# Performance work log

Measured on AMD Instinct MI355X. Metric: run time of the kernel, lower is better.

The kernel has to match this reference:

```python
import jax, jax.numpy as jnp
import numpy as np

H = 3584        # hidden_size
NH = 16         # num_attention_heads
HD = 256        # head_dim
NKV = 8         # num_key_value_heads
GROUPS = NH // NKV
B, S = 2, 2048
SOFTCAP = 50.0
SCALE = 256.0 ** -0.5   # query_pre_attn_scalar ** -0.5
ROPE_BASE = 10000.0
NEG = -1e9


def _rotate_half(x):
    x1, x2 = jnp.split(x, 2, axis=-1)
    return jnp.concatenate([-x2, x1], axis=-1)


def _apply_rope(x, cos, sin):
    # x: [b, h, s, d]; cos/sin: [s, d]
    return x * cos[None, None] + _rotate_half(x) * sin[None, None]


def setup_inputs() -> dict:
    key = jax.random.key(0)
    k1, k2, k3, k4, k5 = jax.random.split(key, 5)
    hidden_states = jax.random.normal(k1, (B, S, H), dtype=jnp.float32)
    # additive causal mask [1, 1, S, S]
    causal = jnp.tril(jnp.ones((S, S), dtype=bool))
    attention_mask = jnp.where(causal, 0.0, NEG).astype(jnp.float32)[None, None]
    Wq = jax.random.normal(k2, (H, NH * HD), dtype=jnp.float32) * 0.02
    Wk = jax.random.normal(k3, (H, NKV * HD), dtype=jnp.float32) * 0.02
    Wv = jax.random.normal(k4, (H, NKV * HD), dtype=jnp.float32) * 0.02
    Wo = jax.random.normal(k5, (NH * HD, H), dtype=jnp.float32) * 0.02
    return {"hidden_states": hidden_states, "attention_mask": attention_mask,
            "Wq": Wq, "Wk": Wk, "Wv": Wv, "Wo": Wo}


def reference(hidden_states, attention_mask, Wq, Wk, Wv, Wo):
    b, s, _ = hidden_states.shape
    q = (hidden_states @ Wq).reshape(b, s, NH, HD).transpose(0, 2, 1, 3)   # [b,nh,s,d]
    k = (hidden_states @ Wk).reshape(b, s, NKV, HD).transpose(0, 2, 1, 3)  # [b,nkv,s,d]
    v = (hidden_states @ Wv).reshape(b, s, NKV, HD).transpose(0, 2, 1, 3)

    # RoPE (HF-style: freqs duplicated, rotate_half)
    pos = jnp.arange(s, dtype=jnp.float32)
    inv_freq = 1.0 / (ROPE_BASE ** (jnp.arange(0, HD, 2, dtype=jnp.float32) / HD))
    freqs = pos[:, None] * inv_freq[None, :]          # [s, d/2]
    emb = jnp.concatenate([freqs, freqs], axis=-1)    # [s, d]
    cos, sin = jnp.cos(emb), jnp.sin(emb)
    q = _apply_rope(q, cos, sin)
    k = _apply_rope(k, cos, sin)

    # repeat_kv for GQA
    k = jnp.repeat(k, GROUPS, axis=1)  # [b,nh,s,d]
    v = jnp.repeat(v, GROUPS, axis=1)

    scores = jnp.einsum('bhsd,bhtd->bhst', q, k) * SCALE
    # tanh logit softcapping
    scores = jnp.tanh(scores / SOFTCAP) * SOFTCAP
    scores = scores + attention_mask
    probs = jax.nn.softmax(scores.astype(jnp.float32), axis=-1).astype(q.dtype)
    out = jnp.einsum('bhst,bhtd->bhsd', probs, v)
    out = out.transpose(0, 2, 1, 3).reshape(b, s, NH * HD)
    return out @ Wo
```

## Files before the change

kernel.cpp:

```cpp
#include <hip/hip_runtime.h>
#include <cstdint>
#include <cstddef>

typedef __bf16 bf16x8 __attribute__((ext_vector_type(8)));
typedef unsigned short u16x8 __attribute__((ext_vector_type(8)));
typedef float  f32x4  __attribute__((ext_vector_type(4)));
typedef unsigned short u16;

#define GLDS16(GP, LP) __builtin_amdgcn_global_load_lds( \
    (const __attribute__((address_space(1))) void*)(GP), \
    (__attribute__((address_space(3))) void*)(LP), 16, 0, 0)

__device__ __forceinline__ float b2f(u16 u) {
  unsigned int x = ((unsigned int)u) << 16;
  return __builtin_bit_cast(float, x);
}
__device__ __forceinline__ u16 f2b(float f) {
  unsigned int u = __builtin_bit_cast(unsigned int, f);
  unsigned int r = (u + 0x7fffu + ((u >> 16) & 1u)) >> 16;
  return (u16)r;
}

constexpr int Bc  = 2;
constexpr int Sc  = 2048;
constexpr int Hc  = 3584;
constexpr int NHc = 16;
constexpr int HDc = 256;
constexpr int NKV = 8;
constexpr int QD  = NHc * HDc;
constexpr int QS  = 8192;
constexpr float SCALE   = 0.0625f;
constexpr float CAP     = 50.0f;
constexpr float INV_CAP = 1.0f / 50.0f;

__device__ __forceinline__ float softcap(float raw) {
  float y = raw * (SCALE * INV_CAP);
  float a = __builtin_fabsf(y);
  float e = __expf(-2.0f * a);
  float t = (1.0f - e) * __builtin_amdgcn_rcpf(1.0f + e);
  return copysignf(t, y) * CAP;
}

__global__ void rope_table_k(float* __restrict__ cosT, float* __restrict__ sinT) {
  int idx = blockIdx.x * 256 + threadIdx.x;
  int s = idx >> 7, i = idx & 127;
  float inv = expf((float)i * -0.0719557841560639f);
  float ang = (float)s * inv;
  cosT[idx] = cosf(ang);
  sinT[idx] = sinf(ang);
}

__global__ void cvt_f32_bf16(const float4* __restrict__ in, ushort4* __restrict__ out, int n4) {
  int i = blockIdx.x * 256 + threadIdx.x;
  int st = gridDim.x * 256;
  for (; i < n4; i += st) {
    float4 v = in[i];
    ushort4 u;
    u.x = f2b(v.x); u.y = f2b(v.y); u.z = f2b(v.z); u.w = f2b(v.w);
    out[i] = u;
  }
}

__global__ void transpose_cvt(const float* __restrict__ in, u16* __restrict__ out, int R, int C) {
  __shared__ float t[32][33];
  int c0 = blockIdx.x * 32, r0 = blockIdx.y * 32;
  int tx = threadIdx.x, ty = threadIdx.y;
#pragma unroll
  for (int i = 0; i < 4; i++)
    t[ty + i * 8][tx] = in[(size_t)(r0 + ty + i * 8) * C + c0 + tx];
  __syncthreads();
#pragma unroll
  for (int i = 0; i < 4; i++)
    out[(size_t)(c0 + ty + i * 8) * R + r0 + tx] = f2b(t[tx][ty + i * 8]);
}

__global__ void transpose_v(const u16* __restrict__ QKV, u16* __restrict__ Vt) {
  __shared__ u16 t[32][33];
  int b = blockIdx.z >> 3, kvh = blockIdx.z & 7;
  int s0 = blockIdx.x * 32, d0 = blockIdx.y * 32;
  int tx = threadIdx.x, ty = threadIdx.y;
#pragma unroll
  for (int i = 0; i < 4; i++)
    t[ty + i * 8][tx] = QKV[(size_t)(b * Sc + s0 + ty + i * 8) * QS + 6144 + kvh * HDc + d0 + tx];
  __syncthreads();
#pragma unroll
  for (int i = 0; i < 4; i++)
    Vt[(size_t)((b * NKV + kvh) * HDc + d0 + ty + i * 8) * Sc + s0 + tx] = t[tx][ty + i * 8];
}

template <int NH>
__global__ void rope_apply(u16* __restrict__ X, const float* __restrict__ cosT,
                           const float* __restrict__ sinT) {
  constexpr int LS = (NH == 16) ? 4 : 3;
  int idx = blockIdx.x * 256 + threadIdx.x;
  const int i4 = (idx & 31) << 2;
  const int h = (idx >> 5) & (NH - 1);
  const int row = idx >> (5 + LS);
  const int s = row & (Sc - 1);
  u16* p = X + (size_t)row * QS + h * 256 + i4;
  ushort4 lo = *(const ushort4*)p;
  ushort4 hi = *(const ushort4*)(p + 128);
  float4 c = *(const float4*)(cosT + s * 128 + i4);
  float4 sn = *(const float4*)(sinT + s * 128 + i4);
  ushort4 nlo, nhi;
  { float xl = b2f(lo.x), xh = b2f(hi.x);
    nlo.x = f2b(xl * c.x - xh * sn.x); nhi.x = f2b(xh * c.x + xl * sn.x); }
  { float xl = b2f(lo.y), xh = b2f(hi.y);
    nlo.y = f2b(xl * c.y - xh * sn.y); nhi.y = f2b(xh * c.y + xl * sn.y); }
  { float xl = b2f(lo.z), xh = b2f(hi.z);
    nlo.z = f2b(xl * c.z - xh * sn.z); nhi.z = f2b(xh * c.z + xl * sn.z); }
  { float xl = b2f(lo.w), xh = b2f(hi.w);
    nlo.w = f2b(xl * c.w - xh * sn.w); nhi.w = f2b(xh * c.w + xl * sn.w); }
  *(ushort4*)p = nlo;
  *(ushort4*)(p + 128) = nhi;
}

template <typename OT>
__global__ __launch_bounds__(512, 1) void gemm256(const u16* __restrict__ A,
                                                  const u16* __restrict__ Bt,
                                                  OT* __restrict__ C,
                                                  int M, int N, int K, int GM) {
  __shared__ alignas(16) u16 As[2][256 * 64];
  __shared__ alignas(16) u16 Bs[2][256 * 64];
  const int nwg = gridDim.x;
  const int cpx = nwg >> 3;
  const int wgid = (blockIdx.x & 7) * cpx + (blockIdx.x >> 3);
  const int GN = nwg / GM;
  const int width = 8 * GN;
  const int grp = wgid / width;
  const int rem = wgid - grp * width;
  const int m0 = (grp * 8 + (rem & 7)) * 256;
  const int n0 = (rem >> 3) * 256;
  const int tid = threadIdx.x;
  const int lane = tid & 63;
  const int w = tid >> 6;
  const int wm = w >> 2, wn = w & 3;
  const int lg = lane >> 4, lr = lane & 15;
  const int nkt = K >> 6;

  auto STAGE = [&](int buf, int kt) {
    const int k0 = kt * 64;
#pragma unroll
    for (int i = 0; i < 4; i++) {
      int c = i * 512 + tid;
      int row = c >> 3, slot = c & 7;
      GLDS16(A + (size_t)(m0 + row) * K + k0 + (slot ^ (row & 7)) * 8,
             (char*)As[buf] + c * 16);
    }
#pragma unroll
    for (int i = 0; i < 4; i++) {
      int c = i * 512 + tid;
      int row = c >> 3, slot = c & 7;
      GLDS16(Bt + (size_t)(n0 + row) * K + k0 + (slot ^ (row & 7)) * 8,
             (char*)Bs[buf] + c * 16);
    }
  };

  f32x4 acc[8][4] = {};

  STAGE(0, 0);
  STAGE(1, 1);
  asm volatile("s_waitcnt vmcnt(8)" ::: "memory");
  __builtin_amdgcn_sched_barrier(0);
  __builtin_amdgcn_s_barrier();

  for (int kt = 0; kt < nkt; ++kt) {
    const int buf = kt & 1;
    bf16x8 bfr[4][2], af[4][2], af2[4][2];
#pragma unroll
    for (int j = 0; j < 4; j++)
#pragma unroll
      for (int ks = 0; ks < 2; ks++) {
        int row = wn * 64 + j * 16 + lr;
        bfr[j][ks] = *(const bf16x8*)&Bs[buf][row * 64 + ((ks * 4 + lg) ^ (row & 7)) * 8];
      }
#pragma unroll
    for (int i = 0; i < 4; i++)
#pragma unroll
      for (int ks = 0; ks < 2; ks++) {
        int row = wm * 128 + i * 16 + lr;
        af[i][ks] = *(const bf16x8*)&As[buf][row * 64 + ((ks * 4 + lg) ^ (row & 7)) * 8];
      }
#pragma unroll
    for (int i = 0; i < 4; i++)
#pragma unroll
      for (int ks = 0; ks < 2; ks++) {
        int row = wm * 128 + 64 + i * 16 + lr;
        af2[i][ks] = *(const bf16x8*)&As[buf][row * 64 + ((ks * 4 + lg) ^ (row & 7)) * 8];
      }
    __builtin_amdgcn_s_setprio(1);
#pragma unroll
    for (int i = 0; i < 4; i++)
#pragma unroll
      for (int j = 0; j < 4; j++)
#pragma unroll
        for (int ks = 0; ks < 2; ks++)
          acc[i][j] = __builtin_amdgcn_mfma_f32_16x16x32_bf16(
              af[i][ks], bfr[j][ks], acc[i][j], 0, 0, 0);
    __builtin_amdgcn_s_setprio(0);
    asm volatile("s_waitcnt vmcnt(0) lgkmcnt(0)" ::: "memory");
    __builtin_amdgcn_sched_barrier(0);
    __builtin_amdgcn_s_barrier();
    if (kt + 2 < nkt) STAGE(buf, kt + 2);
    __builtin_amdgcn_s_setprio(1);
#pragma unroll
    for (int i = 0; i < 4; i++)
#pragma unroll
      for (int j = 0; j < 4; j++)
#pragma unroll
        for (int ks = 0; ks < 2; ks++)
          acc[4 + i][j] = __builtin_amdgcn_mfma_f32_16x16x32_bf16(
              af2[i][ks], bfr[j][ks], acc[4 + i][j], 0, 0, 0);
    __builtin_amdgcn_s_setprio(0);
  }

#pragma unroll
  for (int i = 0; i < 8; i++) {
    const int row = m0 + wm * 128 + i * 16 + lg * 4;
#pragma unroll
    for (int j = 0; j < 4; j++) {
      const int col = n0 + wn * 64 + j * 16 + lr;
#pragma unroll
      for (int r = 0; r < 4; r++) {
        if constexpr (sizeof(OT) == 2)
          C[(size_t)(row + r) * N + col] = f2b(acc[i][j][r]);
        else
          C[(size_t)(row + r) * N + col] = acc[i][j][r];
      }
    }
  }
}

__global__ __launch_bounds__(512) void attn_fwd(const u16* __restrict__ QKV,
                                                const u16* __restrict__ Vt,
                                                const float* __restrict__ cosT,
                                                const float* __restrict__ sinT,
                                                u16* __restrict__ AO) {
  constexpr int KVB = 32;
  __shared__ alignas(16) u16 Ks[2][KVB * 256];
  __shared__ alignas(16) u16 Vs[2][256 * KVB];
  __shared__ alignas(16) u16 Ps[8][16][40];
  const int bx = blockIdx.x, h = blockIdx.y, b = blockIdx.z;
  const int qt = b ? (15 - bx) : bx;
  const int q0 = qt * 128;
  const int kvh = h >> 1;
  const int tid = threadIdx.x, w = tid >> 6, lane = tid & 63;
  const int lg = lane >> 4, lr = lane & 15;
  const int myrow = q0 + w * 16 + lr;

  u16x8 qr[8];
  {
    const u16* qp = QKV + (size_t)(b * Sc + myrow) * QS + h * HDc + lg * 8;
#pragma unroll
    for (int kk = 0; kk < 8; kk++) qr[kk] = *(const u16x8*)(qp + kk * 32);
    const float* ct = cosT + myrow * 128 + lg * 8;
    const float* st = sinT + myrow * 128 + lg * 8;
#pragma unroll
    for (int kk = 0; kk < 4; kk++)
#pragma unroll
      for (int q4 = 0; q4 < 2; q4++) {
        float4 c = *(const float4*)(ct + kk * 32 + q4 * 4);
        float4 s = *(const float4*)(st + kk * 32 + q4 * 4);
#pragma unroll
        for (int e = 0; e < 4; e++) {
          int ei = q4 * 4 + e;
          float cc = (&c.x)[e], ss = (&s.x)[e];
          float lo = b2f(qr[kk][ei]), hi = b2f(qr[kk + 4][ei]);
          qr[kk][ei]     = f2b(lo * cc - hi * ss);
          qr[kk + 4][ei] = f2b(hi * cc + lo * ss);
        }
      }
  }
  bf16x8 qf[8];
#pragma unroll
  for (int kk = 0; kk < 8; kk++) qf[kk] = __builtin_bit_cast(bf16x8, qr[kk]);

  f32x4 o[16] = {};
  float m_r[4], l_r[4];
#pragma unroll
  for (int r = 0; r < 4; r++) { m_r[r] = -1e30f; l_r[r] = 0.0f; }
  const int my_qrow = q0 + w * 16 + lg * 4;
  const int wave_min_row = q0 + w * 16;
  const int wave_max_row = q0 + w * 16 + 15;

  const u16* kbase = QKV + (size_t)(b * Sc) * QS + 4096 + kvh * HDc;
  const u16* vbase = Vt + (size_t)((b * NKV + kvh) * HDc) * Sc;

  auto STAGE = [&](int buf, int t0) {
#pragma unroll
    for (int i = 0; i < 2; i++) {
      int c = i * 512 + tid;
      int row = c >> 5, slot = c & 31;
      GLDS16(kbase + (size_t)(t0 + row) * QS + (slot ^ (row & 7)) * 8,
             (char*)Ks[buf] + c * 16);
    }
#pragma unroll
    for (int i = 0; i < 2; i++) {
      int c = i * 512 + tid;
      int d = c >> 2, slot = c & 3;
      GLDS16(vbase + (size_t)d * Sc + t0 + (slot ^ (d & 3)) * 8,
             (char*)Vs[buf] + c * 16);
    }
  };

  const int nt = 4 * qt + 4;
  int cur = 0;
  STAGE(0, 0);
  for (int ti = 0; ti < nt; ++ti) {
    const int t0 = ti * 32;
    if (ti + 1 < nt) {
      STAGE(cur ^ 1, t0 + 32);
      asm volatile("s_waitcnt vmcnt(4)" ::: "memory");
    } else {
      asm volatile("s_waitcnt vmcnt(0)" ::: "memory");
    }
    __builtin_amdgcn_sched_barrier(0);
    __builtin_amdgcn_s_barrier();

    if (t0 <= wave_max_row) {
      const u16* KsT = Ks[cur];
      const u16* VsT = Vs[cur];

      f32x4 sc[2];
#pragma unroll
      for (int j = 0; j < 2; j++) {
        f32x4 a = {0.f, 0.f, 0.f, 0.f};
        const int row = j * 16 + lr;
#pragma unroll
        for (int kk = 0; kk < 8; kk++) {
          int s0 = (kk * 4 + lg) ^ (lr & 7);
          bf16x8 kf = *(const bf16x8*)&KsT[row * 256 + s0 * 8];
          a = __builtin_amdgcn_mfma_f32_16x16x32_bf16(qf[kk], kf, a, 0, 0, 0);
        }
        sc[j] = a;
      }

      float tmax[4] = {-1e30f, -1e30f, -1e30f, -1e30f};
      if (t0 + 31 > wave_min_row) {
#pragma unroll
        for (int j = 0; j < 2; j++)
#pragma unroll
          for (int r = 0; r < 4; r++) {
            float x = softcap(sc[j][r]);
            if (t0 + j * 16 + lr > my_qrow + r) x = -1e9f;
            sc[j][r] = x;
            tmax[r] = fmaxf(tmax[r], x);
          }
      } else {
#pragma unroll
        for (int j = 0; j < 2; j++)
#pragma unroll
          for (int r = 0; r < 4; r++) {
            float x = softcap(sc[j][r]);
            sc[j][r] = x;
            tmax[r] = fmaxf(tmax[r], x);
          }
      }
#pragma unroll
      for (int xm = 1; xm < 16; xm <<= 1)
#pragma unroll
        for (int r = 0; r < 4; r++) tmax[r] = fmaxf(tmax[r], __shfl_xor(tmax[r], xm, 64));

      bool need = false;
#pragma unroll
      for (int r = 0; r < 4; r++) need |= (tmax[r] > m_r[r] + 8.0f);
      if (__any(need)) {
        float scal[4];
#pragma unroll
        for (int r = 0; r < 4; r++) {
          float mn = fmaxf(m_r[r], tmax[r]);
          scal[r] = __expf(m_r[r] - mn);
          m_r[r] = mn;
          l_r[r] *= scal[r];
        }
#pragma unroll
        for (int df = 0; df < 16; df++)
#pragma unroll
          for (int r = 0; r < 4; r++) o[df][r] *= scal[r];
      }

      float psum[4] = {0.f, 0.f, 0.f, 0.f};
#pragma unroll
      for (int j = 0; j < 2; j++)
#pragma unroll
        for (int r = 0; r < 4; r++) {
          float p = __expf(sc[j][r] - m_r[r]);
          psum[r] += p;
          Ps[w][lg * 4 + r][j * 16 + lr] = f2b(p);
        }
#pragma unroll
      for (int xm = 1; xm < 16; xm <<= 1)
#pragma unroll
        for (int r = 0; r < 4; r++) psum[r] += __shfl_xor(psum[r], xm, 64);
#pragma unroll
      for (int r = 0; r < 4; r++) l_r[r] += psum[r];

      bf16x8 pf = *(const bf16x8*)&Ps[w][lr][lg * 8];
#pragma unroll
      for (int df = 0; df < 16; df++) {
        const int d = df * 16 + lr;
        int s0 = lg ^ (d & 3);
        bf16x8 vf = *(const bf16x8*)&VsT[d * KVB + s0 * 8];
        o[df] = __builtin_amdgcn_mfma_f32_16x16x32_bf16(pf, vf, o[df], 0, 0, 0);
      }
    }

    __builtin_amdgcn_s_barrier();
    cur ^= 1;
  }

  float inv_l[4];
#pragma unroll
  for (int r = 0; r < 4; r++) inv_l[r] = 1.0f / l_r[r];
  u16* op = AO + (size_t)(b * Sc + my_qrow) * QD + h * HDc + lr;
#pragma unroll
  for (int df = 0; df < 16; df++)
#pragma unroll
    for (int r = 0; r < 4; r++)
      op[(size_t)r * QD + df * 16] = f2b(o[df][r] * inv_l[r]);
}

extern "C" void kernel_launch(void* const* d_in, const int* in_sizes, int n_in,
                              void* d_out, int out_size, void* d_ws, size_t ws_size,
                              hipStream_t stream) {
  (void)in_sizes; (void)n_in; (void)out_size; (void)ws_size;
  const float* hs = (const float*)d_in[0];
  const float* Wq = (const float*)d_in[2];
  const float* Wk = (const float*)d_in[3];
  const float* Wv = (const float*)d_in[4];
  const float* Wo = (const float*)d_in[5];
  float* out = (float*)d_out;
  char* ws = (char*)d_ws;

  float* cosT = (float*)(ws + 0);
  float* sinT = (float*)(ws + 1048576);
  u16* hsb    = (u16*)(ws + 2097152);
  u16* Wqkvt  = (u16*)(ws + 31457280);
  u16* Wot    = (u16*)(ws + 90177536);
  u16* QKVb   = (u16*)(ws + 119537664);
  u16* Vtr    = hsb;
  u16* AO     = Wqkvt;

  dim3 tb32x8(32, 8);

  rope_table_k<<<1024, 256, 0, stream>>>(cosT, sinT);
  cvt_f32_bf16<<<2048, 256, 0, stream>>>((const float4*)hs, (ushort4*)hsb, (Bc * Sc * Hc) / 4);
  transpose_cvt<<<dim3(QD / 32, Hc / 32), tb32x8, 0, stream>>>(Wq, Wqkvt, Hc, QD);
  transpose_cvt<<<dim3(2048 / 32, Hc / 32), tb32x8, 0, stream>>>(Wk, Wqkvt + (size_t)4096 * Hc, Hc, 2048);
  transpose_cvt<<<dim3(2048 / 32, Hc / 32), tb32x8, 0, stream>>>(Wv, Wqkvt + (size_t)6144 * Hc, Hc, 2048);
  transpose_cvt<<<dim3(Hc / 32, QD / 32), tb32x8, 0, stream>>>(Wo, Wot, QD, Hc);

  gemm256<u16><<<dim3(16 * 32), 512, 0, stream>>>(hsb, Wqkvt, QKVb, Bc * Sc, QS, Hc, 16);

  rope_apply<8><<<4096, 256, 0, stream>>>(QKVb + 4096, cosT, sinT);
  transpose_v<<<dim3(Sc / 32, HDc / 32, Bc * NKV), tb32x8, 0, stream>>>(QKVb, Vtr);

  attn_fwd<<<dim3(16, NHc, Bc), 512, 0, stream>>>(QKVb, Vtr, cosT, sinT, AO);

  gemm256<float><<<dim3(16 * 14), 512, 0, stream>>>(AO, Wot, out, Bc * Sc, Hc, QD, 16);
}
```

Measured before the change: 666.8 us.

## Use 64-wide KV tiles with a single LDS buffer in attention

Doubles the attention KV tile from 32 to 64 keys, which halves the loop trip count and the barriers per tile and issues two PV MFMAs per tile. The K/V tiles drop from double to single buffering, so each iteration loads its tile and waits for it before computing; there is no longer any prefetch overlap inside a block. The P scratch buffer is widened to 64 columns and XOR-swizzled to avoid LDS bank conflicts, and the V swizzle is extended to 8 slots. Total LDS use stays about the same, so hiding load latency now depends on other resident blocks.

```diff
diff --git a/kernel.cpp b/kernel.cpp
--- a/kernel.cpp
+++ b/kernel.cpp
@@ -236,10 +236,10 @@
                                                 const float* __restrict__ cosT,
                                                 const float* __restrict__ sinT,
                                                 u16* __restrict__ AO) {
-  constexpr int KVB = 32;
-  __shared__ alignas(16) u16 Ks[2][KVB * 256];
-  __shared__ alignas(16) u16 Vs[2][256 * KVB];
-  __shared__ alignas(16) u16 Ps[8][16][40];
+  constexpr int KVB = 64;
+  __shared__ alignas(16) u16 Ks[KVB * 256];
+  __shared__ alignas(16) u16 Vs[256 * KVB];
+  __shared__ alignas(16) u16 Ps[8][16][64];
   const int bx = blockIdx.x, h = blockIdx.y, b = blockIdx.z;
   const int qt = b ? (15 - bx) : bx;
   const int q0 = qt * 128;
@@ -286,59 +286,48 @@
   const u16* kbase = QKV + (size_t)(b * Sc) * QS + 4096 + kvh * HDc;
   const u16* vbase = Vt + (size_t)((b * NKV + kvh) * HDc) * Sc;
 
-  auto STAGE = [&](int buf, int t0) {
-#pragma unroll
-    for (int i = 0; i < 2; i++) {
+  auto STAGE = [&](int t0) {
+#pragma unroll
+    for (int i = 0; i < 4; i++) {
       int c = i * 512 + tid;
       int row = c >> 5, slot = c & 31;
-      GLDS16(kbase + (size_t)(t0 + row) * QS + (slot ^ (row & 7)) * 8,
-             (char*)Ks[buf] + c * 16);
-    }
-#pragma unroll
-    for (int i = 0; i < 2; i++) {
+      GLDS16(kbase + (size_t)(t0 + row) * QS + (slot ^ (row & 7)) * 8, (char*)Ks + c * 16);
+    }
+#pragma unroll
+    for (int i = 0; i < 4; i++) {
       int c = i * 512 + tid;
-      int d = c >> 2, slot = c & 3;
-      GLDS16(vbase + (size_t)d * Sc + t0 + (slot ^ (d & 3)) * 8,
-             (char*)Vs[buf] + c * 16);
+      int d = c >> 3, slot = c & 7;
+      GLDS16(vbase + (size_t)d * Sc + t0 + (slot ^ (d & 7)) * 8, (char*)Vs + c * 16);
     }
   };
 
-  const int nt = 4 * qt + 4;
-  int cur = 0;
-  STAGE(0, 0);
+  const int nt = 2 * qt + 2;
   for (int ti = 0; ti < nt; ++ti) {
-    const int t0 = ti * 32;
-    if (ti + 1 < nt) {
-      STAGE(cur ^ 1, t0 + 32);
-      asm volatile("s_waitcnt vmcnt(4)" ::: "memory");
-    } else {
-      asm volatile("s_waitcnt vmcnt(0)" ::: "memory");
-    }
+    const int t0 = ti * 64;
+    STAGE(t0);
+    asm volatile("s_waitcnt vmcnt(0)" ::: "memory");
     __builtin_amdgcn_sched_barrier(0);
     __builtin_amdgcn_s_barrier();
 
     if (t0 <= wave_max_row) {
-      const u16* KsT = Ks[cur];
-      const u16* VsT = Vs[cur];
-
-      f32x4 sc[2];
-#pragma unroll
-      for (int j = 0; j < 2; j++) {
+      f32x4 sc[4];
+#pragma unroll
+      for (int j = 0; j < 4; j++) {
         f32x4 a = {0.f, 0.f, 0.f, 0.f};
         const int row = j * 16 + lr;
 #pragma unroll
         for (int kk = 0; kk < 8; kk++) {
           int s0 = (kk * 4 + lg) ^ (lr & 7);
-          bf16x8 kf = *(const bf16x8*)&KsT[row * 256 + s0 * 8];
+          bf16x8 kf = *(const bf16x8*)&Ks[row * 256 + s0 * 8];
           a = __builtin_amdgcn_mfma_f32_16x16x32_bf16(qf[kk], kf, a, 0, 0, 0);
         }
         sc[j] = a;
       }
 
       float tmax[4] = {-1e30f, -1e30f, -1e30f, -1e30f};
-      if (t0 + 31 > wave_min_row) {
-#pragma unroll
-        for (int j = 0; j < 2; j++)
+      if (t0 + 63 > wave_min_row) {
+#pragma unroll
+        for (int j = 0; j < 4; j++)
 #pragma unroll
           for (int r = 0; r < 4; r++) {
             float x = softcap(sc[j][r]);
@@ -348,7 +337,7 @@
           }
       } else {
 #pragma unroll
-        for (int j = 0; j < 2; j++)
+        for (int j = 0; j < 4; j++)
 #pragma unroll
           for (int r = 0; r < 4; r++) {
             float x = softcap(sc[j][r]);
@@ -381,12 +370,13 @@
 
       float psum[4] = {0.f, 0.f, 0.f, 0.f};
 #pragma unroll
-      for (int j = 0; j < 2; j++)
+      for (int j = 0; j < 4; j++)
 #pragma unroll
         for (int r = 0; r < 4; r++) {
           float p = __expf(sc[j][r] - m_r[r]);
           psum[r] += p;
-          Ps[w][lg * 4 + r][j * 16 + lr] = f2b(p);
+          int q = lg * 4 + r;
+          Ps[w][q][(j * 16 + lr) ^ ((q & 7) << 3)] = f2b(p);
         }
 #pragma unroll
       for (int xm = 1; xm < 16; xm <<= 1)
@@ -395,18 +385,21 @@
 #pragma unroll
       for (int r = 0; r < 4; r++) l_r[r] += psum[r];
 
-      bf16x8 pf = *(const bf16x8*)&Ps[w][lr][lg * 8];
+      bf16x8 pf0 = *(const bf16x8*)&Ps[w][lr][(lg ^ (lr & 7)) * 8];
+      bf16x8 pf1 = *(const bf16x8*)&Ps[w][lr][((lg ^ 4) ^ (lr & 7)) * 8];
 #pragma unroll
       for (int df = 0; df < 16; df++) {
         const int d = df * 16 + lr;
-        int s0 = lg ^ (d & 3);
-        bf16x8 vf = *(const bf16x8*)&VsT[d * KVB + s0 * 8];
-        o[df] = __builtin_amdgcn_mfma_f32_16x16x32_bf16(pf, vf, o[df], 0, 0, 0);
+        int s0 = lg ^ (d & 7);
+        int s1 = (4 + lg) ^ (d & 7);
+        bf16x8 vf0 = *(const bf16x8*)&Vs[d * KVB + s0 * 8];
+        o[df] = __builtin_amdgcn_mfma_f32_16x16x32_bf16(pf0, vf0, o[df], 0, 0, 0);
+        bf16x8 vf1 = *(const bf16x8*)&Vs[d * KVB + s1 * 8];
+        o[df] = __builtin_amdgcn_mfma_f32_16x16x32_bf16(pf1, vf1, o[df], 0, 0, 0);
       }
     }
 
     __builtin_amdgcn_s_barrier();
-    cur ^= 1;
   }
 
   float inv_l[4];
```

Result: faster. 623.3 us (-6.5%).
